# Kernel tuning notes

Measured on AMD Instinct MI355X. Metric: run time of the kernel, lower is better.

## Reference

```python
import jax, jax.numpy as jnp
import numpy as np

D = 8196        # 4*n_landmark + (n_agents-1)*size_channel + 4
H = 4096        # hidden_size
MLP_HID = 32
OUT = 2 + 128   # 2 + size_channel


def setup_inputs() -> dict:
    key = jax.random.key(0)
    ks = jax.random.split(key, 8)
    s = 0.02
    return {
        "x": jax.random.normal(ks[0], (D,), jnp.float32),
        "h0": jnp.zeros((H,), jnp.float32),
        "c0": jnp.zeros((H,), jnp.float32),
        # LSTM params (PyTorch layout: gates stacked as [i, f, g, o])
        "W_ih": jax.random.normal(ks[1], (4 * H, D), jnp.float32) * s,
        "W_hh": jax.random.normal(ks[2], (4 * H, H), jnp.float32) * s,
        "b_ih": jax.random.normal(ks[3], (4 * H,), jnp.float32) * s,
        "b_hh": jax.random.normal(ks[4], (4 * H,), jnp.float32) * s,
        # MLP: Linear(H,32) -> ReLU -> Linear(32, OUT) -> Sigmoid
        "W1": jax.random.normal(ks[5], (MLP_HID, H), jnp.float32) * s,
        "b1": jnp.zeros((MLP_HID,), jnp.float32),
        "W2": jax.random.normal(ks[6], (OUT, MLP_HID), jnp.float32) * s,
        "b2": jnp.zeros((OUT,), jnp.float32),
    }


def reference(x, h0, c0, W_ih, W_hh, b_ih, b_hh, W1, b1, W2, b2):
    # single LSTM step (batch=1, seq=1), PyTorch gate order i,f,g,o
    gates = W_ih @ x + b_ih + W_hh @ h0 + b_hh            # [4H]
    i, f, g, o = jnp.split(gates, 4)
    i = jax.nn.sigmoid(i)
    f = jax.nn.sigmoid(f)
    g = jnp.tanh(g)
    o = jax.nn.sigmoid(o)
    c = f * c0 + i * g
    h = o * jnp.tanh(c)                                   # [H]
    # MLP head: Linear -> ReLU -> Linear -> Sigmoid, then flatten
    z = jax.nn.relu(W1 @ h + b1)                          # [32]
    out = jax.nn.sigmoid(W2 @ z + b2)                     # [OUT]
    return out
```

## Files before the change

kernel.cpp:

```cpp
#include <hip/hip_runtime.h>
#include <hip/hip_bf16.h>

#define D 8196
#define H 4096
#define MLP_HID 32
#define OUT_N 130
#define ND4 2049
#define NH4 1024

__device__ __forceinline__ float sigmoidf_(float v) {
    return 1.0f / (1.0f + expf(-v));
}

__device__ __forceinline__ float dot4(float4 a, float4 b) {
    return a.x * b.x + a.y * b.y + a.z * b.z + a.w * b.w;
}

__device__ __forceinline__ float wave_reduce(float acc) {
    #pragma unroll
    for (int off = 32; off > 0; off >>= 1)
        acc += __shfl_down(acc, off);
    return acc;
}

__global__ __launch_bounds__(256, 3) void lstm_step_kernel(
    const float* __restrict__ x, const float* __restrict__ h0,
    const float* __restrict__ c0,
    const float* __restrict__ W_ih, const float* __restrict__ W_hh,
    const float* __restrict__ b_ih, const float* __restrict__ b_hh,
    float* __restrict__ h_out)
{
    __shared__ float4 xs[ND4];
    __shared__ float4 hs[NH4];
    __shared__ float gate[4][2];

    const int tid = threadIdx.x;
    {
        const float4* __restrict__ x4 = (const float4*)x;
        const float4* __restrict__ h4 = (const float4*)h0;
        for (int i = tid; i < ND4; i += 256) xs[i] = x4[i];
        for (int i = tid; i < NH4; i += 256) hs[i] = h4[i];
    }
    __syncthreads();

    const int g    = tid >> 6;
    const int lane = tid & 63;
    const int j0   = blockIdx.x * 2;

    #pragma unroll
    for (int rr = 0; rr < 2; ++rr) {
        const size_t r = (size_t)g * H + j0 + rr;
        float a = 0.0f;

        {
            const float4* __restrict__ A = (const float4*)(W_ih + r * D);
            #pragma unroll 8
            for (int it = 0; it < 32; ++it) {
                const int idx = it * 64 + lane;
                a += dot4(A[idx], xs[idx]);
            }
            if (lane == 0)
                a += dot4(A[2048], xs[2048]);
        }
        {
            const float4* __restrict__ B = (const float4*)(W_hh + r * H);
            #pragma unroll 8
            for (int it = 0; it < 16; ++it) {
                const int idx = it * 64 + lane;
                a += dot4(B[idx], hs[idx]);
            }
        }

        a = wave_reduce(a);
        if (lane == 0)
            gate[g][rr] = a + b_ih[r] + b_hh[r];
    }
    __syncthreads();

    if (tid < 2) {
        const int j = j0 + tid;
        const float ig = sigmoidf_(gate[0][tid]);
        const float fg = sigmoidf_(gate[1][tid]);
        const float gg = tanhf(gate[2][tid]);
        const float og = sigmoidf_(gate[3][tid]);
        const float c  = fg * c0[j] + ig * gg;
        h_out[j] = og * tanhf(c);
    }
}

__global__ __launch_bounds__(1024) void mlp_head_kernel(
    const float* __restrict__ h,
    const float* __restrict__ W1, const float* __restrict__ b1,
    const float* __restrict__ W2, const float* __restrict__ b2,
    float* __restrict__ out)
{
    __shared__ float z[MLP_HID];
    const int wave = threadIdx.x >> 6;
    const int lane = threadIdx.x & 63;

    for (int r = wave; r < MLP_HID; r += 16) {
        const float4* __restrict__ Wr = (const float4*)(W1 + (size_t)r * H);
        const float4* __restrict__ h4 = (const float4*)h;
        float acc = 0.0f;
        #pragma unroll 4
        for (int idx = lane; idx < H / 4; idx += 64)
            acc += dot4(Wr[idx], h4[idx]);
        acc = wave_reduce(acc);
        if (lane == 0)
            z[r] = fmaxf(acc + b1[r], 0.0f);
    }
    __syncthreads();

    const int t = threadIdx.x;
    if (t < OUT_N) {
        float acc = b2[t];
        #pragma unroll
        for (int k = 0; k < MLP_HID; ++k)
            acc += W2[t * MLP_HID + k] * z[k];
        out[t] = sigmoidf_(acc);
    }
}

extern "C" void kernel_launch(void* const* d_in, const int* in_sizes, int n_in,
                              void* d_out, int out_size, void* d_ws, size_t ws_size,
                              hipStream_t stream) {
    const float* x    = (const float*)d_in[0];
    const float* h0   = (const float*)d_in[1];
    const float* c0   = (const float*)d_in[2];
    const float* W_ih = (const float*)d_in[3];
    const float* W_hh = (const float*)d_in[4];
    const float* b_ih = (const float*)d_in[5];
    const float* b_hh = (const float*)d_in[6];
    const float* W1   = (const float*)d_in[7];
    const float* b1   = (const float*)d_in[8];
    const float* W2   = (const float*)d_in[9];
    const float* b2   = (const float*)d_in[10];
    float* out = (float*)d_out;

    float* h_ws = (float*)d_ws;

    lstm_step_kernel<<<H / 2, 256, 0, stream>>>(x, h0, c0, W_ih, W_hh, b_ih, b_hh, h_ws);
    mlp_head_kernel<<<1, 1024, 0, stream>>>(h_ws, W1, b1, W2, b2, out);
}
```

Baseline: 162.7 us.

## Use 512-thread LSTM blocks, read h0 from global, split MLP head into two kernels

The LSTM kernel now runs 512-thread blocks, each computing four hidden units instead of two. This halves the grid and the number of times x is staged into shared memory. h0 is no longer copied to shared memory and is read directly from global/cache, which cuts LDS use and allows higher occupancy. The single-block MLP head is split into a 32-block kernel for the first layer and a small output kernel, spreading the W1 reads across CUs at the cost of an extra launch.

```diff
diff --git a/kernel.cpp b/kernel.cpp
--- a/kernel.cpp
+++ b/kernel.cpp
@@ -23,7 +23,7 @@
     return acc;
 }
 
-__global__ __launch_bounds__(256, 3) void lstm_step_kernel(
+__global__ __launch_bounds__(512, 8) void lstm_step_kernel(
     const float* __restrict__ x, const float* __restrict__ h0,
     const float* __restrict__ c0,
     const float* __restrict__ W_ih, const float* __restrict__ W_hh,
@@ -31,30 +31,30 @@
     float* __restrict__ h_out)
 {
     __shared__ float4 xs[ND4];
-    __shared__ float4 hs[NH4];
-    __shared__ float gate[4][2];
+    __shared__ float gate[4][4];
 
     const int tid = threadIdx.x;
     {
         const float4* __restrict__ x4 = (const float4*)x;
-        const float4* __restrict__ h4 = (const float4*)h0;
-        for (int i = tid; i < ND4; i += 256) xs[i] = x4[i];
-        for (int i = tid; i < NH4; i += 256) hs[i] = h4[i];
+        for (int i = tid; i < ND4; i += 512) xs[i] = x4[i];
     }
     __syncthreads();
 
-    const int g    = tid >> 6;
+    const int w    = tid >> 6;
     const int lane = tid & 63;
-    const int j0   = blockIdx.x * 2;
+    const int g    = w & 3;
+    const int p    = w >> 2;
+    const int j0   = blockIdx.x * 4;
 
     #pragma unroll
     for (int rr = 0; rr < 2; ++rr) {
-        const size_t r = (size_t)g * H + j0 + rr;
+        const int u = 2 * p + rr;
+        const size_t r = (size_t)g * H + j0 + u;
         float a = 0.0f;
 
         {
             const float4* __restrict__ A = (const float4*)(W_ih + r * D);
-            #pragma unroll 8
+            #pragma unroll 4
             for (int it = 0; it < 32; ++it) {
                 const int idx = it * 64 + lane;
                 a += dot4(A[idx], xs[idx]);
@@ -64,20 +64,21 @@
         }
         {
             const float4* __restrict__ B = (const float4*)(W_hh + r * H);
-            #pragma unroll 8
+            const float4* __restrict__ h4 = (const float4*)h0;
+            #pragma unroll 4
             for (int it = 0; it < 16; ++it) {
                 const int idx = it * 64 + lane;
-                a += dot4(B[idx], hs[idx]);
+                a += dot4(B[idx], h4[idx]);
             }
         }
 
         a = wave_reduce(a);
         if (lane == 0)
-            gate[g][rr] = a + b_ih[r] + b_hh[r];
+            gate[g][u] = a + b_ih[r] + b_hh[r];
     }
     __syncthreads();
 
-    if (tid < 2) {
+    if (tid < 4) {
         const int j = j0 + tid;
         const float ig = sigmoidf_(gate[0][tid]);
         const float fg = sigmoidf_(gate[1][tid]);
@@ -88,35 +89,40 @@
     }
 }
 
-__global__ __launch_bounds__(1024) void mlp_head_kernel(
+__global__ __launch_bounds__(64) void mlp_z_kernel(
     const float* __restrict__ h,
     const float* __restrict__ W1, const float* __restrict__ b1,
+    float* __restrict__ z)
+{
+    const int r    = blockIdx.x;
+    const int lane = threadIdx.x;
+    const float4* __restrict__ Wr = (const float4*)(W1 + (size_t)r * H);
+    const float4* __restrict__ h4 = (const float4*)h;
+    float acc = 0.0f;
+    #pragma unroll 4
+    for (int it = 0; it < 16; ++it) {
+        const int idx = it * 64 + lane;
+        acc += dot4(Wr[idx], h4[idx]);
+    }
+    acc = wave_reduce(acc);
+    if (lane == 0)
+        z[r] = fmaxf(acc + b1[r], 0.0f);
+}
+
+__global__ __launch_bounds__(192) void mlp_out_kernel(
+    const float* __restrict__ z,
     const float* __restrict__ W2, const float* __restrict__ b2,
     float* __restrict__ out)
 {
-    __shared__ float z[MLP_HID];
-    const int wave = threadIdx.x >> 6;
-    const int lane = threadIdx.x & 63;
-
-    for (int r = wave; r < MLP_HID; r += 16) {
-        const float4* __restrict__ Wr = (const float4*)(W1 + (size_t)r * H);
-        const float4* __restrict__ h4 = (const float4*)h;
-        float acc = 0.0f;
-        #pragma unroll 4
-        for (int idx = lane; idx < H / 4; idx += 64)
-            acc += dot4(Wr[idx], h4[idx]);
-        acc = wave_reduce(acc);
-        if (lane == 0)
-            z[r] = fmaxf(acc + b1[r], 0.0f);
-    }
+    __shared__ float zs[MLP_HID];
+    if (threadIdx.x < MLP_HID) zs[threadIdx.x] = z[threadIdx.x];
     __syncthreads();
-
     const int t = threadIdx.x;
     if (t < OUT_N) {
         float acc = b2[t];
         #pragma unroll
         for (int k = 0; k < MLP_HID; ++k)
-            acc += W2[t * MLP_HID + k] * z[k];
+            acc += W2[t * MLP_HID + k] * zs[k];
         out[t] = sigmoidf_(acc);
     }
 }
@@ -138,7 +144,9 @@
     float* out = (float*)d_out;
 
     float* h_ws = (float*)d_ws;
+    float* z_ws = (float*)((char*)d_ws + 16384);
 
-    lstm_step_kernel<<<H / 2, 256, 0, stream>>>(x, h0, c0, W_ih, W_hh, b_ih, b_hh, h_ws);
-    mlp_head_kernel<<<1, 1024, 0, stream>>>(h_ws, W1, b1, W2, b2, out);
+    lstm_step_kernel<<<H / 4, 512, 0, stream>>>(x, h0, c0, W_ih, W_hh, b_ih, b_hh, h_ws);
+    mlp_z_kernel<<<MLP_HID, 64, 0, stream>>>(h_ws, W1, b1, z_ws);
+    mlp_out_kernel<<<1, 192, 0, stream>>>(z_ws, W2, b2, out);
 }
```

Measured after the change: 153.1 us. 5.9% less time.
